# Performance work log

Hardware: AMD Instinct MI355X
Metric: run time of the kernel (lower is better)

The kernel has to match this reference:

```python
import jax, jax.numpy as jnp
import numpy as np

HEADS = 8

def _proj(x, W, b):
    # 1x1 conv == per-pixel linear: x [B,C,H,W], W [O,C], b [O]
    return jnp.einsum('bchw,oc->bohw', x, W) + b[None, :, None, None]

def setup_inputs() -> dict:
    key = jax.random.key(0)
    ks = jax.random.split(key, 9)
    B, C, H, W = 8, 256, 32, 32
    s = C ** -0.5
    return {
        'x':  jax.random.normal(ks[0], (B, C, H, W), jnp.float32),
        'Wq': jax.random.normal(ks[1], (C, C), jnp.float32) * s,
        'bq': jax.random.normal(ks[2], (C,), jnp.float32) * 0.02,
        'Wk': jax.random.normal(ks[3], (C, C), jnp.float32) * s,
        'bk': jax.random.normal(ks[4], (C,), jnp.float32) * 0.02,
        'Wv': jax.random.normal(ks[5], (C, C), jnp.float32) * s,
        'bv': jax.random.normal(ks[6], (C,), jnp.float32) * 0.02,
        'Wm': jax.random.normal(ks[7], (C, C), jnp.float32) * s,
        'bm': jax.random.normal(ks[8], (C,), jnp.float32) * 0.02,
    }

def reference(x, Wq, bq, Wk, bk, Wv, bv, Wm, bm):
    B, C, H, W = x.shape
    h = HEADS
    hd = C // h
    scale = hd ** -0.5

    def to_heads(t):
        # [B,C,H,W] -> [B,h,hd,H,W] -> [B,h,HW,hd]
        t = t.reshape(B, h, hd, H, W)
        return t.transpose(0, 1, 3, 4, 2).reshape(B, h, H * W, hd)

    q = to_heads(_proj(x, Wq, bq))
    k = to_heads(_proj(x, Wk, bk))
    v = to_heads(_proj(x, Wv, bv))

    attn = jax.nn.softmax(jnp.einsum('bhnd,bhmd->bhnm', q, k) * scale, axis=-1)
    out = jnp.einsum('bhnm,bhmd->bhnd', attn, v)          # [B,h,HW,hd]
    # torch: view(B,h,H,W,hd).permute(0,4,1,2,3).view(B,C,H,W) => channel = d*h + head
    out = out.reshape(B, h, H, W, hd).transpose(0, 4, 1, 2, 3).reshape(B, C, H, W)
    return _proj(out, Wm, bm)
```

## Files before the change

### kernel.cpp

```cpp
#include <hip/hip_runtime.h>
#include <cstdint>
#include <cstddef>


#define NB 8
#define NC 256
#define NP 1024
#define NHD 8
#define HD 32

typedef short bf16x8 __attribute__((ext_vector_type(8)));
typedef float f32x4 __attribute__((ext_vector_type(4)));
typedef float f32x16 __attribute__((ext_vector_type(16)));

#define SCLLOG 0.25505654356918f

#define F32X16_ZERO (f32x16){0.f,0.f,0.f,0.f,0.f,0.f,0.f,0.f,0.f,0.f,0.f,0.f,0.f,0.f,0.f,0.f}

__device__ __forceinline__ unsigned cvt_pk_bf16(float a, float b) {
  unsigned r;
  asm("v_cvt_pk_bf16_f32 %0, %1, %2" : "=v"(r) : "v"(a), "v"(b));
  return r;
}
__device__ __forceinline__ unsigned short f2b1(float a) {
  return (unsigned short)cvt_pk_bf16(a, a);
}

__global__ __launch_bounds__(256) void prep_kernel(
    const float* __restrict__ Wq, const float* __restrict__ Wk,
    const float* __restrict__ Wv, const float* __restrict__ Wm,
    const float* __restrict__ x, unsigned short* __restrict__ Wb,
    unsigned short* __restrict__ xt) {
  __shared__ float sx[64][65];
  int bx = blockIdx.x, tid = threadIdx.x;
  if (bx < 128) {
    int idx = (bx * 256 + tid) * 8;
    const float* src; int off;
    if (idx < 65536)       { src = Wq; off = idx; }
    else if (idx < 131072) { src = Wk; off = idx - 65536; }
    else if (idx < 196608) { src = Wv; off = idx - 131072; }
    else                   { src = Wm; off = idx - 196608; }
    float4 lo = *(const float4*)(src + off);
    float4 hi = *(const float4*)(src + off + 4);
    union { unsigned u[4]; bf16x8 v; } o;
    o.u[0] = cvt_pk_bf16(lo.x, lo.y); o.u[1] = cvt_pk_bf16(lo.z, lo.w);
    o.u[2] = cvt_pk_bf16(hi.x, hi.y); o.u[3] = cvt_pk_bf16(hi.z, hi.w);
    *(bf16x8*)(Wb + idx) = o.v;
  } else {
    int bi = bx - 128;
    int b = bi >> 6, rest = bi & 63;
    int ct = (rest & 3) * 64, pt = (rest >> 2) * 64;
    const float* xb = x + ((size_t)(b * NC + ct)) * NP + pt;
    int pr = (tid & 15) * 4, cr = tid >> 4;
#pragma unroll
    for (int i = 0; i < 4; i++) {
      float4 v = *(const float4*)(xb + (size_t)(cr + i * 16) * NP + pr);
      sx[cr + i*16][pr]   = v.x; sx[cr + i*16][pr+1] = v.y;
      sx[cr + i*16][pr+2] = v.z; sx[cr + i*16][pr+3] = v.w;
    }
    __syncthreads();
    int pl = tid >> 3, cc = (tid & 7) * 8;
#pragma unroll
    for (int j = 0; j < 2; j++) {
      int p = pl + j * 32;
      union { unsigned u[4]; bf16x8 v; } o;
#pragma unroll
      for (int u = 0; u < 4; u++)
        o.u[u] = cvt_pk_bf16(sx[cc + 2*u][p], sx[cc + 2*u + 1][p]);
      *(bf16x8*)(xt + ((size_t)b * NP + pt + p) * NC + ct + cc) = o.v;
    }
  }
}

__global__ __launch_bounds__(256) void qkv_kernel(
    const unsigned short* __restrict__ Wb,
    const float* __restrict__ bq, const float* __restrict__ bk,
    const float* __restrict__ bv,
    const unsigned short* __restrict__ xt,
    unsigned short* __restrict__ qt, unsigned short* __restrict__ kt,
    unsigned short* __restrict__ vt) {
  int proj = blockIdx.z, b = blockIdx.y, bx = blockIdx.x;
  int ot = (bx & 3) * 64, pt = (bx >> 2) * 64;
  int tid = threadIdx.x, wave = tid >> 6, lane = tid & 63;
  int l15 = lane & 15, quad = lane >> 4;
  int oW = ot + (wave & 1) * 32, pW = pt + (wave >> 1) * 32;
  const unsigned short* W = Wb + (size_t)proj * 65536;
  const float* bias = (proj == 0) ? bq : (proj == 1) ? bk : bv;
  float sc = (proj == 0) ? SCLLOG : 1.0f;
  const unsigned short* A0 = W + (size_t)(oW + l15) * NC + quad * 8;
  const unsigned short* B0 = xt + ((size_t)b * NP + pW + l15) * NC + quad * 8;
  f32x4 acc[2][2];
#pragma unroll
  for (int i = 0; i < 2; i++)
#pragma unroll
    for (int j = 0; j < 2; j++) acc[i][j] = (f32x4){0.f, 0.f, 0.f, 0.f};
#pragma unroll
  for (int c0 = 0; c0 < NC; c0 += 32) {
    bf16x8 a0 = *(const bf16x8*)(A0 + c0);
    bf16x8 a1 = *(const bf16x8*)(A0 + 16 * NC + c0);
    bf16x8 b0 = *(const bf16x8*)(B0 + c0);
    bf16x8 b1 = *(const bf16x8*)(B0 + 16 * NC + c0);
    acc[0][0] = __builtin_amdgcn_mfma_f32_16x16x32_bf16(a0, b0, acc[0][0], 0, 0, 0);
    acc[0][1] = __builtin_amdgcn_mfma_f32_16x16x32_bf16(a0, b1, acc[0][1], 0, 0, 0);
    acc[1][0] = __builtin_amdgcn_mfma_f32_16x16x32_bf16(a1, b0, acc[1][0], 0, 0, 0);
    acc[1][1] = __builtin_amdgcn_mfma_f32_16x16x32_bf16(a1, b1, acc[1][1], 0, 0, 0);
  }
  unsigned short* qk = (proj == 0) ? qt : kt;
#pragma unroll
  for (int rh = 0; rh < 2; rh++) {
    int od0 = oW + rh * 16 + quad * 4;
    float b0 = bias[od0], b1 = bias[od0+1], b2 = bias[od0+2], b3 = bias[od0+3];
#pragma unroll
    for (int ch = 0; ch < 2; ch++) {
      float v0 = acc[rh][ch][0] + b0, v1 = acc[rh][ch][1] + b1;
      float v2 = acc[rh][ch][2] + b2, v3 = acc[rh][ch][3] + b3;
      int p = pW + ch * 16 + l15;
      if (proj < 2) {
        int h2 = od0 >> 5, d0 = od0 & 31;
        uint2 pk;
        pk.x = cvt_pk_bf16(v0 * sc, v1 * sc);
        pk.y = cvt_pk_bf16(v2 * sc, v3 * sc);
        size_t idx = ((size_t)(b * NHD + h2) * NP + p) * HD + d0;
        *(uint2*)(qk + idx) = pk;
      } else {
        size_t base = ((size_t)b * NC + od0) * NP + p;
        vt[base]          = f2b1(v0);
        vt[base +     NP] = f2b1(v1);
        vt[base + 2 * NP] = f2b1(v2);
        vt[base + 3 * NP] = f2b1(v3);
      }
    }
  }
}

__global__ __launch_bounds__(256, 4) void attn_kernel(
    const unsigned short* __restrict__ qt, const unsigned short* __restrict__ kt,
    const unsigned short* __restrict__ vt, unsigned short* __restrict__ at) {
  int tid = threadIdx.x, wave = tid >> 6, lane = tid & 63;
  int l31 = lane & 31, hi = lane >> 5;
  int half = wave >> 1, wsub = wave & 1;
  int bh = blockIdx.y, b = bh >> 3, h = bh & 7;
  int n0 = blockIdx.x * 64 + wsub * 32;

  __shared__ float Comb[2][64][17];
  __shared__ float Linv[2][32];

  const unsigned short* qp = qt + ((size_t)bh * NP + n0 + l31) * HD + hi * 8;
  bf16x8 qf0 = *(const bf16x8*)(qp);
  bf16x8 qf1 = *(const bf16x8*)(qp + 16);

  const unsigned short* kp = kt + ((size_t)bh * NP + l31) * HD + hi * 8;
  const unsigned short* vp = vt + ((size_t)(b * NC + h * HD + l31)) * NP + hi * 8;

  f32x16 oacc = F32X16_ZERO;
  f32x4 la = (f32x4){0.f, 0.f, 0.f, 0.f};

  int mbase = half * 512;
  bf16x8 kf0 = *(const bf16x8*)(kp + (size_t)mbase * HD);
  bf16x8 kf1 = *(const bf16x8*)(kp + (size_t)mbase * HD + 16);
  bf16x8 vf0 = *(const bf16x8*)(vp + mbase);
  bf16x8 vf1 = *(const bf16x8*)(vp + mbase + 16);

  for (int m0 = mbase; m0 < mbase + 512; m0 += 32) {
    f32x16 s = __builtin_amdgcn_mfma_f32_32x32x16_bf16(kf0, qf0, F32X16_ZERO, 0, 0, 0);
    s = __builtin_amdgcn_mfma_f32_32x32x16_bf16(kf1, qf1, s, 0, 0, 0);
    bf16x8 nk0 = *(const bf16x8*)(kp + (size_t)(m0 + 32) * HD);
    bf16x8 nk1 = *(const bf16x8*)(kp + (size_t)(m0 + 32) * HD + 16);
    bf16x8 nv0 = *(const bf16x8*)(vp + m0 + 32);
    bf16x8 nv1 = *(const bf16x8*)(vp + m0 + 48);
    float p[16];
#pragma unroll
    for (int r = 0; r < 16; r++) p[r] = __builtin_amdgcn_exp2f(s[r]);
#pragma unroll
    for (int r = 0; r < 16; r++) la[r & 3] += p[r];
    unsigned w0 = cvt_pk_bf16(p[0],  p[1]),  w1 = cvt_pk_bf16(p[2],  p[3]);
    unsigned w2 = cvt_pk_bf16(p[4],  p[5]),  w3 = cvt_pk_bf16(p[6],  p[7]);
    unsigned w4 = cvt_pk_bf16(p[8],  p[9]),  w5 = cvt_pk_bf16(p[10], p[11]);
    unsigned w6 = cvt_pk_bf16(p[12], p[13]), w7 = cvt_pk_bf16(p[14], p[15]);
    asm("v_permlane32_swap_b32 %0, %1" : "+v"(w0), "+v"(w2));
    asm("v_permlane32_swap_b32 %0, %1" : "+v"(w1), "+v"(w3));
    asm("v_permlane32_swap_b32 %0, %1" : "+v"(w4), "+v"(w6));
    asm("v_permlane32_swap_b32 %0, %1" : "+v"(w5), "+v"(w7));
    union { unsigned u[4]; bf16x8 v; } pa0, pa1;
    pa0.u[0] = w0; pa0.u[1] = w1; pa0.u[2] = w2; pa0.u[3] = w3;
    pa1.u[0] = w4; pa1.u[1] = w5; pa1.u[2] = w6; pa1.u[3] = w7;
    oacc = __builtin_amdgcn_mfma_f32_32x32x16_bf16(pa0.v, vf0, oacc, 0, 0, 0);
    oacc = __builtin_amdgcn_mfma_f32_32x32x16_bf16(pa1.v, vf1, oacc, 0, 0, 0);
    kf0 = nk0; kf1 = nk1; vf0 = nv0; vf1 = nv1;
  }

  float lsum = (la[0] + la[1]) + (la[2] + la[3]);
  lsum += __shfl_xor(lsum, 32, 64);

  if (half == 1) {
    float* Cb = &Comb[wsub][lane][0];
#pragma unroll
    for (int r = 0; r < 16; r++) Cb[r] = oacc[r];
    Cb[16] = lsum;
  }
  __syncthreads();
  if (half == 0) {
    const float* Cb = &Comb[wsub][lane][0];
#pragma unroll
    for (int r = 0; r < 16; r++) oacc[r] += Cb[r];
    lsum += Cb[16];
    if (hi == 0) Linv[wsub][l31] = 1.0f / lsum;
    unsigned short* ab = at + (size_t)b * NP * NC + (size_t)(l31 * 8 + h);
#pragma unroll
    for (int r = 0; r < 16; r++) {
      int crow = (r & 3) + 8 * (r >> 2) + 4 * hi;
      float iv = Linv[wsub][crow];
      ab[(size_t)(n0 + crow) * NC] = f2b1(oacc[r] * iv);
    }
  }
}

__global__ __launch_bounds__(256) void mproj_kernel(
    const unsigned short* __restrict__ Wmb, const float* __restrict__ bm,
    const unsigned short* __restrict__ at, float* __restrict__ out) {
  int b = blockIdx.y, bx = blockIdx.x;
  int ot = (bx & 3) * 64, pt = (bx >> 2) * 64;
  int tid = threadIdx.x, wave = tid >> 6, lane = tid & 63;
  int l15 = lane & 15, quad = lane >> 4;
  int oW = ot + (wave & 1) * 32, pW = pt + (wave >> 1) * 32;
  const unsigned short* A0 = Wmb + (size_t)(oW + l15) * NC + quad * 8;
  const unsigned short* B0 = at + ((size_t)b * NP + pW + l15) * NC + quad * 8;
  f32x4 acc[2][2];
#pragma unroll
  for (int i = 0; i < 2; i++)
#pragma unroll
    for (int j = 0; j < 2; j++) acc[i][j] = (f32x4){0.f, 0.f, 0.f, 0.f};
#pragma unroll
  for (int c0 = 0; c0 < NC; c0 += 32) {
    bf16x8 a0 = *(const bf16x8*)(A0 + c0);
    bf16x8 a1 = *(const bf16x8*)(A0 + 16 * NC + c0);
    bf16x8 b0 = *(const bf16x8*)(B0 + c0);
    bf16x8 b1 = *(const bf16x8*)(B0 + 16 * NC + c0);
    acc[0][0] = __builtin_amdgcn_mfma_f32_16x16x32_bf16(a0, b0, acc[0][0], 0, 0, 0);
    acc[0][1] = __builtin_amdgcn_mfma_f32_16x16x32_bf16(a0, b1, acc[0][1], 0, 0, 0);
    acc[1][0] = __builtin_amdgcn_mfma_f32_16x16x32_bf16(a1, b0, acc[1][0], 0, 0, 0);
    acc[1][1] = __builtin_amdgcn_mfma_f32_16x16x32_bf16(a1, b1, acc[1][1], 0, 0, 0);
  }
#pragma unroll
  for (int rh = 0; rh < 2; rh++) {
    int od0 = oW + rh * 16 + quad * 4;
    float b0 = bm[od0], b1 = bm[od0+1], b2 = bm[od0+2], b3 = bm[od0+3];
#pragma unroll
    for (int ch = 0; ch < 2; ch++) {
      int p = pW + ch * 16 + l15;
      size_t base = ((size_t)b * NC + od0) * NP + p;
      out[base]          = acc[rh][ch][0] + b0;
      out[base +     NP] = acc[rh][ch][1] + b1;
      out[base + 2 * NP] = acc[rh][ch][2] + b2;
      out[base + 3 * NP] = acc[rh][ch][3] + b3;
    }
  }
}

extern "C" void kernel_launch(void* const* d_in, const int* in_sizes, int n_in,
                              void* d_out, int out_size, void* d_ws, size_t ws_size,
                              hipStream_t stream) {
  (void)in_sizes; (void)n_in; (void)out_size; (void)ws_size;
  const float* x  = (const float*)d_in[0];
  const float* Wq = (const float*)d_in[1];
  const float* bq = (const float*)d_in[2];
  const float* Wk = (const float*)d_in[3];
  const float* bk = (const float*)d_in[4];
  const float* Wv = (const float*)d_in[5];
  const float* bv = (const float*)d_in[6];
  const float* Wm = (const float*)d_in[7];
  const float* bm = (const float*)d_in[8];
  float* out = (float*)d_out;
  char* ws = (char*)d_ws;

  unsigned short* xt = (unsigned short*)(ws);
  unsigned short* Wb = (unsigned short*)(ws + (4u << 20));
  unsigned short* qt = (unsigned short*)(ws + (4u << 20) + (512u << 10));
  unsigned short* kt = (unsigned short*)(ws + (8u << 20) + (512u << 10));
  unsigned short* vt = (unsigned short*)(ws + (12u << 20) + (512u << 10));
  unsigned short* at = (unsigned short*)(ws + (16u << 20) + (512u << 10));

  prep_kernel<<<640, 256, 0, stream>>>(Wq, Wk, Wv, Wm, x, Wb, xt);
  qkv_kernel<<<dim3(64, 8, 3), 256, 0, stream>>>(Wb, bq, bk, bv, xt, qt, kt, vt);
  attn_kernel<<<dim3(16, 64), 256, 0, stream>>>(qt, kt, vt, at);
  mproj_kernel<<<dim3(64, 8), 256, 0, stream>>>(Wb + 3 * 65536, bm, at, out);
}
```

Baseline: 135.9 us.

## Give each attention wave two query tiles over a quarter of keys

After: 131.0 us. -3.6%, faster.

```diff
diff --git a/kernel.cpp b/kernel.cpp
--- a/kernel.cpp
+++ b/kernel.cpp
@@ -133,84 +133,109 @@
   }
 }
 
-__global__ __launch_bounds__(256, 4) void attn_kernel(
+__global__ __launch_bounds__(256, 3) void attn_kernel(
     const unsigned short* __restrict__ qt, const unsigned short* __restrict__ kt,
     const unsigned short* __restrict__ vt, unsigned short* __restrict__ at) {
   int tid = threadIdx.x, wave = tid >> 6, lane = tid & 63;
   int l31 = lane & 31, hi = lane >> 5;
-  int half = wave >> 1, wsub = wave & 1;
   int bh = blockIdx.y, b = bh >> 3, h = bh & 7;
-  int n0 = blockIdx.x * 64 + wsub * 32;
-
-  __shared__ float Comb[2][64][17];
+  int n0 = blockIdx.x * 64;
+
+  __shared__ float Comb[3][64][35];
   __shared__ float Linv[2][32];
 
-  const unsigned short* qp = qt + ((size_t)bh * NP + n0 + l31) * HD + hi * 8;
-  bf16x8 qf0 = *(const bf16x8*)(qp);
-  bf16x8 qf1 = *(const bf16x8*)(qp + 16);
+  const unsigned short* qpa = qt + ((size_t)bh * NP + n0 + l31) * HD + hi * 8;
+  bf16x8 qa0 = *(const bf16x8*)(qpa);
+  bf16x8 qa1 = *(const bf16x8*)(qpa + 16);
+  bf16x8 qb0 = *(const bf16x8*)(qpa + 32 * HD);
+  bf16x8 qb1 = *(const bf16x8*)(qpa + 32 * HD + 16);
 
   const unsigned short* kp = kt + ((size_t)bh * NP + l31) * HD + hi * 8;
   const unsigned short* vp = vt + ((size_t)(b * NC + h * HD + l31)) * NP + hi * 8;
 
-  f32x16 oacc = F32X16_ZERO;
-  f32x4 la = (f32x4){0.f, 0.f, 0.f, 0.f};
-
-  int mbase = half * 512;
+  f32x16 oa = F32X16_ZERO, ob = F32X16_ZERO;
+  f32x4 la = (f32x4){0.f, 0.f, 0.f, 0.f}, lb = (f32x4){0.f, 0.f, 0.f, 0.f};
+
+  int mbase = wave * 256;
   bf16x8 kf0 = *(const bf16x8*)(kp + (size_t)mbase * HD);
   bf16x8 kf1 = *(const bf16x8*)(kp + (size_t)mbase * HD + 16);
   bf16x8 vf0 = *(const bf16x8*)(vp + mbase);
   bf16x8 vf1 = *(const bf16x8*)(vp + mbase + 16);
 
-  for (int m0 = mbase; m0 < mbase + 512; m0 += 32) {
-    f32x16 s = __builtin_amdgcn_mfma_f32_32x32x16_bf16(kf0, qf0, F32X16_ZERO, 0, 0, 0);
-    s = __builtin_amdgcn_mfma_f32_32x32x16_bf16(kf1, qf1, s, 0, 0, 0);
+  for (int m0 = mbase; m0 < mbase + 256; m0 += 32) {
     bf16x8 nk0 = *(const bf16x8*)(kp + (size_t)(m0 + 32) * HD);
     bf16x8 nk1 = *(const bf16x8*)(kp + (size_t)(m0 + 32) * HD + 16);
     bf16x8 nv0 = *(const bf16x8*)(vp + m0 + 32);
     bf16x8 nv1 = *(const bf16x8*)(vp + m0 + 48);
-    float p[16];
-#pragma unroll
-    for (int r = 0; r < 16; r++) p[r] = __builtin_amdgcn_exp2f(s[r]);
-#pragma unroll
-    for (int r = 0; r < 16; r++) la[r & 3] += p[r];
-    unsigned w0 = cvt_pk_bf16(p[0],  p[1]),  w1 = cvt_pk_bf16(p[2],  p[3]);
-    unsigned w2 = cvt_pk_bf16(p[4],  p[5]),  w3 = cvt_pk_bf16(p[6],  p[7]);
-    unsigned w4 = cvt_pk_bf16(p[8],  p[9]),  w5 = cvt_pk_bf16(p[10], p[11]);
-    unsigned w6 = cvt_pk_bf16(p[12], p[13]), w7 = cvt_pk_bf16(p[14], p[15]);
-    asm("v_permlane32_swap_b32 %0, %1" : "+v"(w0), "+v"(w2));
-    asm("v_permlane32_swap_b32 %0, %1" : "+v"(w1), "+v"(w3));
-    asm("v_permlane32_swap_b32 %0, %1" : "+v"(w4), "+v"(w6));
-    asm("v_permlane32_swap_b32 %0, %1" : "+v"(w5), "+v"(w7));
-    union { unsigned u[4]; bf16x8 v; } pa0, pa1;
-    pa0.u[0] = w0; pa0.u[1] = w1; pa0.u[2] = w2; pa0.u[3] = w3;
-    pa1.u[0] = w4; pa1.u[1] = w5; pa1.u[2] = w6; pa1.u[3] = w7;
-    oacc = __builtin_amdgcn_mfma_f32_32x32x16_bf16(pa0.v, vf0, oacc, 0, 0, 0);
-    oacc = __builtin_amdgcn_mfma_f32_32x32x16_bf16(pa1.v, vf1, oacc, 0, 0, 0);
+    f32x16 sa = __builtin_amdgcn_mfma_f32_32x32x16_bf16(kf0, qa0, F32X16_ZERO, 0, 0, 0);
+    f32x16 sb = __builtin_amdgcn_mfma_f32_32x32x16_bf16(kf0, qb0, F32X16_ZERO, 0, 0, 0);
+    sa = __builtin_amdgcn_mfma_f32_32x32x16_bf16(kf1, qa1, sa, 0, 0, 0);
+    sb = __builtin_amdgcn_mfma_f32_32x32x16_bf16(kf1, qb1, sb, 0, 0, 0);
+    float pa[16], pb[16];
+#pragma unroll
+    for (int r = 0; r < 16; r++) pa[r] = __builtin_amdgcn_exp2f(sa[r]);
+#pragma unroll
+    for (int r = 0; r < 16; r++) pb[r] = __builtin_amdgcn_exp2f(sb[r]);
+#pragma unroll
+    for (int r = 0; r < 16; r++) { la[r & 3] += pa[r]; lb[r & 3] += pb[r]; }
+    unsigned a0 = cvt_pk_bf16(pa[0],  pa[1]),  a1 = cvt_pk_bf16(pa[2],  pa[3]);
+    unsigned a2 = cvt_pk_bf16(pa[4],  pa[5]),  a3 = cvt_pk_bf16(pa[6],  pa[7]);
+    unsigned a4 = cvt_pk_bf16(pa[8],  pa[9]),  a5 = cvt_pk_bf16(pa[10], pa[11]);
+    unsigned a6 = cvt_pk_bf16(pa[12], pa[13]), a7 = cvt_pk_bf16(pa[14], pa[15]);
+    asm("v_permlane32_swap_b32 %0, %1" : "+v"(a0), "+v"(a2));
+    asm("v_permlane32_swap_b32 %0, %1" : "+v"(a1), "+v"(a3));
+    asm("v_permlane32_swap_b32 %0, %1" : "+v"(a4), "+v"(a6));
+    asm("v_permlane32_swap_b32 %0, %1" : "+v"(a5), "+v"(a7));
+    unsigned b0 = cvt_pk_bf16(pb[0],  pb[1]),  b1 = cvt_pk_bf16(pb[2],  pb[3]);
+    unsigned b2 = cvt_pk_bf16(pb[4],  pb[5]),  b3 = cvt_pk_bf16(pb[6],  pb[7]);
+    unsigned b4 = cvt_pk_bf16(pb[8],  pb[9]),  b5 = cvt_pk_bf16(pb[10], pb[11]);
+    unsigned b6 = cvt_pk_bf16(pb[12], pb[13]), b7 = cvt_pk_bf16(pb[14], pb[15]);
+    asm("v_permlane32_swap_b32 %0, %1" : "+v"(b0), "+v"(b2));
+    asm("v_permlane32_swap_b32 %0, %1" : "+v"(b1), "+v"(b3));
+    asm("v_permlane32_swap_b32 %0, %1" : "+v"(b4), "+v"(b6));
+    asm("v_permlane32_swap_b32 %0, %1" : "+v"(b5), "+v"(b7));
+    union { unsigned u[4]; bf16x8 v; } fa0, fa1, fb0, fb1;
+    fa0.u[0] = a0; fa0.u[1] = a1; fa0.u[2] = a2; fa0.u[3] = a3;
+    fa1.u[0] = a4; fa1.u[1] = a5; fa1.u[2] = a6; fa1.u[3] = a7;
+    fb0.u[0] = b0; fb0.u[1] = b1; fb0.u[2] = b2; fb0.u[3] = b3;
+    fb1.u[0] = b4; fb1.u[1] = b5; fb1.u[2] = b6; fb1.u[3] = b7;
+    oa = __builtin_amdgcn_mfma_f32_32x32x16_bf16(fa0.v, vf0, oa, 0, 0, 0);
+    oa = __builtin_amdgcn_mfma_f32_32x32x16_bf16(fa1.v, vf1, oa, 0, 0, 0);
+    ob = __builtin_amdgcn_mfma_f32_32x32x16_bf16(fb0.v, vf0, ob, 0, 0, 0);
+    ob = __builtin_amdgcn_mfma_f32_32x32x16_bf16(fb1.v, vf1, ob, 0, 0, 0);
     kf0 = nk0; kf1 = nk1; vf0 = nv0; vf1 = nv1;
   }
 
-  float lsum = (la[0] + la[1]) + (la[2] + la[3]);
-  lsum += __shfl_xor(lsum, 32, 64);
-
-  if (half == 1) {
-    float* Cb = &Comb[wsub][lane][0];
-#pragma unroll
-    for (int r = 0; r < 16; r++) Cb[r] = oacc[r];
-    Cb[16] = lsum;
+  float lsA = (la[0] + la[1]) + (la[2] + la[3]);
+  float lsB = (lb[0] + lb[1]) + (lb[2] + lb[3]);
+  lsA += __shfl_xor(lsA, 32, 64);
+  lsB += __shfl_xor(lsB, 32, 64);
+
+  if (wave) {
+    float* Cb = &Comb[wave - 1][lane][0];
+#pragma unroll
+    for (int r = 0; r < 16; r++) { Cb[r] = oa[r]; Cb[16 + r] = ob[r]; }
+    Cb[32] = lsA; Cb[33] = lsB;
   }
   __syncthreads();
-  if (half == 0) {
-    const float* Cb = &Comb[wsub][lane][0];
-#pragma unroll
-    for (int r = 0; r < 16; r++) oacc[r] += Cb[r];
-    lsum += Cb[16];
-    if (hi == 0) Linv[wsub][l31] = 1.0f / lsum;
+  if (wave == 0) {
+#pragma unroll
+    for (int w = 0; w < 3; w++) {
+      const float* Cb = &Comb[w][lane][0];
+#pragma unroll
+      for (int r = 0; r < 16; r++) { oa[r] += Cb[r]; ob[r] += Cb[16 + r]; }
+      lsA += Cb[32]; lsB += Cb[33];
+    }
+    if (hi == 0) {
+      Linv[0][l31] = 1.0f / lsA;
+      Linv[1][l31] = 1.0f / lsB;
+    }
     unsigned short* ab = at + (size_t)b * NP * NC + (size_t)(l31 * 8 + h);
 #pragma unroll
     for (int r = 0; r < 16; r++) {
       int crow = (r & 3) + 8 * (r >> 2) + 4 * hi;
-      float iv = Linv[wsub][crow];
-      ab[(size_t)(n0 + crow) * NC] = f2b1(oacc[r] * iv);
+      ab[(size_t)(n0 + crow) * NC]      = f2b1(oa[r] * Linv[0][crow]);
+      ab[(size_t)(n0 + 32 + crow) * NC] = f2b1(ob[r] * Linv[1][crow]);
     }
   }
 }
```
